# Kernel optimization log

Hardware: AMD Instinct MI355X
Metric: run time of the kernel (lower is better)

Reference implementation:

```python
import jax, jax.numpy as jnp
import numpy as np

EPS = 1e-06
LOG_BIAS = 1.0  # config.fire_log_bias


def setup_inputs() -> dict:
    key = jax.random.key(0)
    ks = jax.random.split(key, 5)
    S, H, W = 2048, 12, 32
    x = jax.random.normal(ks[0], (1, S, 768), dtype=jnp.float32)
    w1 = jax.random.normal(ks[1], (W, 1), dtype=jnp.float32) * 0.5
    b1 = jax.random.normal(ks[2], (W,), dtype=jnp.float32) * 0.1
    w2 = jax.random.normal(ks[3], (H, W), dtype=jnp.float32) * 0.2
    b2 = jax.random.normal(ks[4], (H,), dtype=jnp.float32) * 0.1
    c = jnp.float32(0.1)            # fire_init_c, trainable
    L_multiplier = jnp.float32(1.0)  # trainable
    init_L = jnp.float32(512.0)      # non-trainable buffer
    return {"x": x, "w1": w1, "b1": b1, "w2": w2, "b2": b2,
            "c": c, "L_multiplier": L_multiplier, "init_L": init_L}


def reference(x, w1, b1, w2, b2, c, L_multiplier, init_L):
    S = x.shape[1]
    pos = jnp.arange(S, dtype=jnp.float32)
    rel = pos[:, None] - pos[None, :]                      # [S, S]
    abs_rel = jnp.abs(rel) + EPS
    threshold = jnp.abs(L_multiplier * init_L)
    pos_norm = jnp.maximum(pos, threshold)[:, None] + EPS  # [S, 1]
    log_rel = jnp.log(abs_rel * c + LOG_BIAS + EPS)        # [S, S]
    log_norm = jnp.log(jnp.abs(c * pos_norm) + LOG_BIAS + EPS)  # [S, 1]
    nd = log_rel / log_norm                                # [S, S]
    # tiny MLP: Linear(1,W) -> ReLU -> Linear(W,H)
    h = jax.nn.relu(nd[..., None] * w1[:, 0] + b1)         # [S, S, W]
    bias = jnp.einsum('stw,hw->hst', h, w2) + b2[:, None, None]  # [H, S, S]
    return bias[None]                                      # [1, H, S, S]
```

## Files before the change

### kernel.cpp

```cpp
#include <hip/hip_runtime.h>
#include <math.h>


#define SDIM 2048
#define WDIM 32
#define HDIM 12
#define NK 33
#define EPSF 1e-6f
#define LOGB 1.0f

#define WS_T 0
#define WS_AB 64
#define WS_TOTAL (64 + 2 * NK * HDIM)

__global__ __launch_bounds__(512) void fire_precompute(
    const float* __restrict__ w1, const float* __restrict__ b1,
    const float* __restrict__ w2, const float* __restrict__ b2,
    float* __restrict__ ws)
{
    __shared__ float traw[WDIM], w1s[WDIM], b1s[WDIM];
    __shared__ int rnk[WDIM], neg[WDIM];
    const int tid = threadIdx.x;

    if (tid < WDIM) {
        float a = w1[tid], b = b1[tid];
        w1s[tid] = a; b1s[tid] = b;
        float t; int isneg;
        if (a > 0.f)      { t = -b / a; isneg = 0; }
        else if (a < 0.f) { t = -b / a; isneg = 1; }
        else {
            t = (b > 0.f) ? -INFINITY : INFINITY; isneg = 0;
        }
        traw[tid] = t; neg[tid] = isneg;
    }
    __syncthreads();

    if (tid < WDIM) {
        float t = traw[tid];
        int r = 0;
        for (int v = 0; v < WDIM; ++v) {
            float tv = traw[v];
            if (tv < t || (tv == t && v < tid)) r++;
        }
        rnk[tid] = r;
        ws[WS_T + r] = t;
    } else if (tid < 64) {
        ws[WS_T + tid] = INFINITY;
    }
    __syncthreads();

    if (tid < NK * HDIM) {
        const int k = tid % NK;
        const int h = tid / NK;
        float a = 0.f, bb = 0.f;
        for (int w = 0; w < WDIM; ++w) {
            const bool active = neg[w] ? (rnk[w] >= k) : (rnk[w] < k);
            if (active) {
                float w2v = w2[h * WDIM + w];
                a  += w2v * w1s[w];
                bb += w2v * b1s[w];
            }
        }
        bb += b2[h];
        ws[WS_AB + (k * HDIM + h) * 2 + 0] = a;
        ws[WS_AB + (k * HDIM + h) * 2 + 1] = bb;
    }
}

__global__ __launch_bounds__(512) void fire_main(
    const float* __restrict__ ws,
    const float* __restrict__ cptr, const float* __restrict__ lmptr,
    const float* __restrict__ ilptr, float* __restrict__ out)
{
    __shared__ float sT[64];
    __shared__ float sAB[2 * NK * HDIM];
    const int tid = threadIdx.x;

    if (tid < 64) sT[tid] = ws[WS_T + tid];
    for (int idx = tid; idx < 2 * NK * HDIM; idx += 512) sAB[idx] = ws[WS_AB + idx];
    __syncthreads();

    const int i = blockIdx.x;
    const float c   = cptr[0];
    const float thr = fabsf(lmptr[0] * ilptr[0]);
    const float pn  = fmaxf((float)i, thr) + EPSF;
    const float inv_ln = 1.0f / logf(fabsf(c * pn) + LOGB + EPSF);

    const int j0 = tid * 4;
    float nd[4];
    int kk[4];
    #pragma unroll
    for (int e = 0; e < 4; ++e) {
        int j = j0 + e;
        int dd = i - j; if (dd < 0) dd = -dd;
        float ar = (float)dd + EPSF;
        float x  = fmaf(ar, c, LOGB + EPSF);
        float ndv = logf(x) * inv_ln;
        nd[e] = ndv;
        int k = 0;
        if (ndv > sT[k + 31]) k += 32;
        if (ndv > sT[k + 15]) k += 16;
        if (ndv > sT[k + 7])  k += 8;
        if (ndv > sT[k + 3])  k += 4;
        if (ndv > sT[k + 1])  k += 2;
        if (ndv > sT[k])      k += 1;
        kk[e] = k;
    }

    const size_t base = (size_t)i * SDIM + (size_t)j0;
    #pragma unroll
    for (int h = 0; h < HDIM; ++h) {
        float4 v;
        float* vp = &v.x;
        #pragma unroll
        for (int e = 0; e < 4; ++e) {
            int idx = (kk[e] * HDIM + h) * 2;
            vp[e] = fmaf(sAB[idx], nd[e], sAB[idx + 1]);
        }
        *(float4*)(out + (size_t)h * SDIM * SDIM + base) = v;
    }
}

extern "C" void kernel_launch(void* const* d_in, const int* in_sizes, int n_in,
                              void* d_out, int out_size, void* d_ws, size_t ws_size,
                              hipStream_t stream)
{
    const float* w1 = (const float*)d_in[1];
    const float* b1 = (const float*)d_in[2];
    const float* w2 = (const float*)d_in[3];
    const float* b2 = (const float*)d_in[4];
    const float* c  = (const float*)d_in[5];
    const float* lm = (const float*)d_in[6];
    const float* il = (const float*)d_in[7];
    float* ws  = (float*)d_ws;
    float* out = (float*)d_out;

    fire_precompute<<<1, 512, 0, stream>>>(w1, b1, w2, b2, ws);
    fire_main<<<SDIM, 512, 0, stream>>>(ws, c, lm, il, out);
}
```

Baseline: 219.2 us.

## Precompute log tables and fold normalizer into thresholds and slopes; nontemporal stores

The precompute kernel now also fills per-distance log tables and per-row log-norm and its inverse using extra blocks. The main kernel drops its per-element logf. It looks up log_rel from shared memory, scales the breakpoint thresholds by the row's log-norm, and folds the inverse norm into the slope coefficients, so no divide or log runs per element. Output stores become nontemporal to avoid polluting cache on the 200MB write. The risk is slightly different rounding from reordering the multiply, plus extra shared-memory loads per block.

```diff
diff --git a/kernel.cpp b/kernel.cpp
--- a/kernel.cpp
+++ b/kernel.cpp
@@ -9,18 +9,37 @@
 #define EPSF 1e-6f
 #define LOGB 1.0f
 
-#define WS_T 0
-#define WS_AB 64
-#define WS_TOTAL (64 + 2 * NK * HDIM)
+typedef float f32x4 __attribute__((ext_vector_type(4)));
+
+#define WS_T   0
+#define WS_AB  64
+#define WS_LR  896
+#define WS_LN  2944
+#define WS_ILN 4992
+#define WS_TOTAL 7040
 
 __global__ __launch_bounds__(512) void fire_precompute(
     const float* __restrict__ w1, const float* __restrict__ b1,
     const float* __restrict__ w2, const float* __restrict__ b2,
-    float* __restrict__ ws)
+    const float* __restrict__ cptr, const float* __restrict__ lmptr,
+    const float* __restrict__ ilptr, float* __restrict__ ws)
 {
+    const int tid = threadIdx.x;
+
+    if (blockIdx.x != 0) {
+        const int d = ((int)blockIdx.x - 1) * 512 + tid;
+        const float c = cptr[0];
+        ws[WS_LR + d] = logf(fmaf((float)d + EPSF, c, LOGB + EPSF));
+        const float thr = fabsf(lmptr[0] * ilptr[0]);
+        const float pn  = fmaxf((float)d, thr) + EPSF;
+        const float ln  = logf(fabsf(c * pn) + LOGB + EPSF);
+        ws[WS_LN  + d] = ln;
+        ws[WS_ILN + d] = 1.0f / ln;
+        return;
+    }
+
     __shared__ float traw[WDIM], w1s[WDIM], b1s[WDIM];
     __shared__ int rnk[WDIM], neg[WDIM];
-    const int tid = threadIdx.x;
 
     if (tid < WDIM) {
         float a = w1[tid], b = b1[tid];
@@ -68,56 +87,55 @@
 }
 
 __global__ __launch_bounds__(512) void fire_main(
-    const float* __restrict__ ws,
-    const float* __restrict__ cptr, const float* __restrict__ lmptr,
-    const float* __restrict__ ilptr, float* __restrict__ out)
+    const float* __restrict__ ws, float* __restrict__ out)
 {
-    __shared__ float sT[64];
+    __shared__ float sTp[64];
     __shared__ float sAB[2 * NK * HDIM];
+    __shared__ __align__(16) float sLR[SDIM];
     const int tid = threadIdx.x;
+    const int i = blockIdx.x;
 
-    if (tid < 64) sT[tid] = ws[WS_T + tid];
-    for (int idx = tid; idx < 2 * NK * HDIM; idx += 512) sAB[idx] = ws[WS_AB + idx];
+    const float ln_i = ws[WS_LN  + i];
+    const float ivl  = ws[WS_ILN + i];
+
+    ((f32x4*)sLR)[tid] = ((const f32x4*)(ws + WS_LR))[tid];
+    if (tid < 64) sTp[tid] = ws[WS_T + tid] * ln_i;
+    for (int idx = tid; idx < 2 * NK * HDIM; idx += 512) {
+        float v = ws[WS_AB + idx];
+        if ((idx & 1) == 0) v *= ivl;
+        sAB[idx] = v;
+    }
     __syncthreads();
 
-    const int i = blockIdx.x;
-    const float c   = cptr[0];
-    const float thr = fabsf(lmptr[0] * ilptr[0]);
-    const float pn  = fmaxf((float)i, thr) + EPSF;
-    const float inv_ln = 1.0f / logf(fabsf(c * pn) + LOGB + EPSF);
-
     const int j0 = tid * 4;
-    float nd[4];
+    float lrv[4];
     int kk[4];
     #pragma unroll
     for (int e = 0; e < 4; ++e) {
         int j = j0 + e;
         int dd = i - j; if (dd < 0) dd = -dd;
-        float ar = (float)dd + EPSF;
-        float x  = fmaf(ar, c, LOGB + EPSF);
-        float ndv = logf(x) * inv_ln;
-        nd[e] = ndv;
+        float x = sLR[dd];
         int k = 0;
-        if (ndv > sT[k + 31]) k += 32;
-        if (ndv > sT[k + 15]) k += 16;
-        if (ndv > sT[k + 7])  k += 8;
-        if (ndv > sT[k + 3])  k += 4;
-        if (ndv > sT[k + 1])  k += 2;
-        if (ndv > sT[k])      k += 1;
+        if (x > sTp[k + 31]) k += 32;
+        if (x > sTp[k + 15]) k += 16;
+        if (x > sTp[k + 7])  k += 8;
+        if (x > sTp[k + 3])  k += 4;
+        if (x > sTp[k + 1])  k += 2;
+        if (x > sTp[k])      k += 1;
         kk[e] = k;
+        lrv[e] = x;
     }
 
     const size_t base = (size_t)i * SDIM + (size_t)j0;
     #pragma unroll
     for (int h = 0; h < HDIM; ++h) {
-        float4 v;
-        float* vp = &v.x;
+        f32x4 v;
         #pragma unroll
         for (int e = 0; e < 4; ++e) {
             int idx = (kk[e] * HDIM + h) * 2;
-            vp[e] = fmaf(sAB[idx], nd[e], sAB[idx + 1]);
+            v[e] = fmaf(sAB[idx], lrv[e], sAB[idx + 1]);
         }
-        *(float4*)(out + (size_t)h * SDIM * SDIM + base) = v;
+        __builtin_nontemporal_store(v, (f32x4*)(out + (size_t)h * SDIM * SDIM + base));
     }
 }
 
@@ -135,6 +153,6 @@
     float* ws  = (float*)d_ws;
     float* out = (float*)d_out;
 
-    fire_precompute<<<1, 512, 0, stream>>>(w1, b1, w2, b2, ws);
-    fire_main<<<SDIM, 512, 0, stream>>>(ws, c, lm, il, out);
+    fire_precompute<<<5, 512, 0, stream>>>(w1, b1, w2, b2, c, lm, il, ws);
+    fire_main<<<SDIM, 512, 0, stream>>>(ws, out);
 }
```

Result: slower. 225.6 us (+2.9%).
